# Kernel optimization log

Hardware: AMD Instinct MI355X
Metric: run time of the kernel (lower is better)

Reference implementation:

```python
import jax, jax.numpy as jnp
from jax import lax
import numpy as np
import math

MAXV = 127.0  # 2**(8-1)-1, signed int8 narrow range

def setup_inputs() -> dict:
    key = jax.random.key(0)
    kx, kw, kb = jax.random.split(key, 3)
    B, Cin, H, W = 32, 128, 56, 56
    Cout, K = 256, 3
    x = jax.random.normal(kx, (B, Cin, H, W), dtype=jnp.float32)
    # kaiming_uniform_(a=sqrt(5)) -> bound = sqrt(6 / ((1+5) * fan_in)) = 1/sqrt(fan_in)
    fan_in = Cin * K * K
    bound = 1.0 / math.sqrt(fan_in)
    weight = jax.random.uniform(kw, (Cout, Cin, K, K), dtype=jnp.float32,
                                minval=-bound, maxval=bound)
    bias = jax.random.uniform(kb, (Cout,), dtype=jnp.float32,
                              minval=-bound, maxval=bound)
    return {"x": x, "weight": weight, "bias": bias}

def _quantize_i8(t):
    """Max-calibrated signed 8-bit quantization (fake_quant=False -> integer output)."""
    amax = jnp.max(jnp.abs(t))
    scale = MAXV / amax
    q = jnp.clip(jnp.round(t * scale), -MAXV, MAXV).astype(jnp.int8)
    return q, scale

def reference(x, weight, bias):
    # quantize activations and weights to int8
    qx, sx = _quantize_i8(x)
    qw, sw = _quantize_i8(weight)
    # exact int8 conv with int32 accumulation (systolic exact path), stride=1, pad=1
    out_i32 = lax.conv_general_dilated(
        qx, qw,
        window_strides=(1, 1),
        padding=((1, 1), (1, 1)),
        dimension_numbers=("NCHW", "OIHW", "NCHW"),
        preferred_element_type=jnp.int32,
    )
    # dequantize and add bias
    out = out_i32.astype(jnp.float32) / (sx * sw)
    return out + bias[None, :, None, None]
```

## Files before the change

kernel.cpp:

```cpp
#include <hip/hip_runtime.h>


#define B_    32
#define CIN   128
#define H_    56
#define W_    56
#define COUT  256
#define HP    58
#define WP    58
#define HWP   (H_*W_)
#define NPIX  (B_*HWP)
#define NCHUNK 18
#define WCHUNK 16384
#define BWIN  24576
#define GSTR  3712

typedef int int4v __attribute__((ext_vector_type(4)));

__device__ __forceinline__ void gld_lds16(const void* g, void* l) {
    __builtin_amdgcn_global_load_lds(
        (const __attribute__((address_space(1))) unsigned int*)g,
        (__attribute__((address_space(3))) unsigned int*)l, 16, 0, 0);
}

__global__ __launch_bounds__(256) void amax_kernel(const float4* __restrict__ x, long n4x,
                                                   const float4* __restrict__ wt, long n4w,
                                                   unsigned* __restrict__ scales) {
    const float4* p; long n4; unsigned* slot; long start, stride;
    if (blockIdx.x < 2048) {
        p = x; n4 = n4x; slot = scales;
        start = (long)blockIdx.x * 256 + threadIdx.x; stride = 2048L * 256;
    } else {
        p = wt; n4 = n4w; slot = scales + 1;
        start = (long)(blockIdx.x - 2048) * 256 + threadIdx.x; stride = 128L * 256;
    }
    float m = 0.f;
    for (long i = start; i < n4; i += stride) {
        float4 v = p[i];
        m = fmaxf(m, fmaxf(fmaxf(fabsf(v.x), fabsf(v.y)), fmaxf(fabsf(v.z), fabsf(v.w))));
    }
    __shared__ float red[256];
    red[threadIdx.x] = m; __syncthreads();
    for (int s = 128; s > 0; s >>= 1) {
        if (threadIdx.x < s) red[threadIdx.x] = fmaxf(red[threadIdx.x], red[threadIdx.x + s]);
        __syncthreads();
    }
    if (threadIdx.x == 0) atomicMax(slot, __float_as_uint(red[0]));
}

__global__ __launch_bounds__(256) void quant_x_kernel(const float* __restrict__ x,
        const unsigned* __restrict__ scales, signed char* __restrict__ xq) {
    const int bh = blockIdx.x;
    const int b = bh / H_, h = bh % H_;
    const float sx = 127.0f / __uint_as_float(scales[0]);
    __shared__ int ldsq[W_ * 33];
    const int tid = threadIdx.x;

    int4 z; z.x = 0; z.y = 0; z.z = 0; z.w = 0;
    int4* prow = (int4*)(xq + ((long)b * HP + h + 1) * WP * CIN);
    if (tid < 8) prow[tid] = z;
    else if (tid < 16) prow[456 + tid - 8] = z;
    if (h == 0) {
        int4* r0 = (int4*)(xq + (long)b * HP * WP * CIN);
        for (int i = tid; i < 464; i += 256) r0[i] = z;
    } else if (h == H_ - 1) {
        int4* rt = (int4*)(xq + ((long)b * HP + 57) * WP * CIN);
        for (int i = tid; i < 464; i += 256) rt[i] = z;
    }

    const int w = tid & 63;
    const int chi = tid >> 6;
    if (w < W_) {
        const float* xb = x + (long)b * CIN * HWP + h * W_ + w;
#pragma unroll
        for (int it = 0; it < 8; ++it) {
            const int c4 = it * 4 + chi;
            int pk = 0;
#pragma unroll
            for (int u = 0; u < 4; ++u) {
                float v = xb[(long)(c4 * 4 + u) * HWP];
                float q = fminf(127.f, fmaxf(-127.f, rintf(v * sx)));
                pk |= ((int)q & 0xff) << (u * 8);
            }
            ldsq[w * 33 + c4] = pk;
        }
    }
    __syncthreads();
    int4* dst = (int4*)(xq + (((long)b * HP + h + 1) * WP + 1) * CIN);
    for (int idx = tid; idx < W_ * 8; idx += 256) {
        const int ww = idx >> 3, c16 = idx & 7;
        int4 v;
        v.x = ldsq[ww * 33 + c16 * 4 + 0];
        v.y = ldsq[ww * 33 + c16 * 4 + 1];
        v.z = ldsq[ww * 33 + c16 * 4 + 2];
        v.w = ldsq[ww * 33 + c16 * 4 + 3];
        dst[ww * 8 + c16] = v;
    }
}

__global__ __launch_bounds__(256) void quant_w_kernel(const float* __restrict__ wt,
        const unsigned* __restrict__ scales, signed char* __restrict__ wq) {
    const int id = blockIdx.x * 256 + threadIdx.x;
    if (id >= COUT * 9 * 32) return;
    const float sw = 127.0f / __uint_as_float(scales[1]);
    const int co = id / 288;
    const int r  = id % 288;
    const int t  = r / 32;
    const int c4 = r % 32;
    int pk = 0;
#pragma unroll
    for (int u = 0; u < 4; ++u) {
        float v = wt[(co * CIN + c4 * 4 + u) * 9 + t];
        float q = fminf(127.f, fmaxf(-127.f, rintf(v * sw)));
        pk |= ((int)q & 0xff) << (u * 8);
    }
    const int k = t * CIN + c4 * 4;
    const int chunk = k >> 6;
    const int o = k & 63;
    *(int*)(wq + (long)chunk * WCHUNK + (co >> 7) * 8192 +
            (o >> 4) * 2048 + (co & 127) * 16 + (o & 15)) = pk;
}

__global__ __launch_bounds__(256, 3) void conv_kernel(
        const signed char* __restrict__ xq, const signed char* __restrict__ wq,
        const float* __restrict__ bias, const unsigned* __restrict__ scales,
        float* __restrict__ out) {
    __shared__ signed char smem[54272];

    const int tid = threadIdx.x;
    const int lane = tid & 63;
    const int wv = tid >> 6;
    const int ln = lane & 15;
    const int g  = lane >> 4;

    const int bid = blockIdx.x;
    const int wg  = (bid & 7) * 224 + (bid >> 3);
    const int pxt = wg >> 1;
    const int cot = wg & 1;
    const int px_blk = pxt * 112;
    const int cotoff = cot * 8192;

    const int b0 = pxt / 28;
    const int h0 = (pxt % 28) * 2;

    const int aoff0 = wv * 1024 + lane * 16;
    const int aoff1 = aoff0 + 4096;

    int px58v[7];
#pragma unroll
    for (int j = 0; j < 7; ++j) {
        const int pl = j * 16 + ln;
        px58v[j] = pl + (pl >= 56 ? 2 : 0);
    }

    const signed char* win = xq + (long)(b0 * HP + h0) * WP * CIN;
    int4v wbuf[8];
#pragma unroll
    for (int k = 0; k < 8; ++k) {
        const int u = tid + k * 256;
        if (u < 1856) wbuf[k] = *(const int4v*)(win + u * 16);
    }
#pragma unroll
    for (int k = 0; k < 8; ++k) {
        const int u = tid + k * 256;
        if (u < 1856)
            *(int4v*)&smem[BWIN + (u & 7) * GSTR + (u >> 3) * 16] = wbuf[k];
    }

#define STAGE_A(c) { const int bf_ = (c) % 3; \
    gld_lds16(wq + (c) * WCHUNK + cotoff + aoff0, &smem[bf_ * 8192 + aoff0]); \
    gld_lds16(wq + (c) * WCHUNK + cotoff + aoff1, &smem[bf_ * 8192 + aoff1]); }

    STAGE_A(0);
    STAGE_A(1);
    asm volatile("s_waitcnt lgkmcnt(0)" ::: "memory");

#define TAP58(c) ((((c) >> 1) / 3) * 58 + (((c) >> 1) % 3))
#define LDA_(i) (*(const int4v*)&smem[buf * 8192 + g * 2048 + (wv * 32 + (i) * 16 + ln) * 16])
#define LDB_(c, j) (*(const int4v*)&smem[BWIN + (((c) & 1) * 4 + g) * GSTR + (px58v[j] + TAP58(c)) * 16])
#define MM(i, j, A, Bv) acc[i][j] = __builtin_amdgcn_mfma_i32_16x16x64_i8(A, Bv, acc[i][j], 0, 0, 0)

#define CHUNK(c, VM) { \
    const int buf = (c) % 3; \
    asm volatile("s_waitcnt vmcnt(" #VM ")\n\ts_barrier" ::: "memory"); \
    if ((c) + 2 < NCHUNK) STAGE_A((c) + 2); \
    int4v Bf0 = LDB_(c, 0), Bf1 = LDB_(c, 1), Bf2 = LDB_(c, 2), Bf3 = LDB_(c, 3); \
    int4v Bf4 = LDB_(c, 4), Bf5 = LDB_(c, 5), Bf6 = LDB_(c, 6); \
    int4v Af0 = LDA_(0), Af1 = LDA_(1); \
    __builtin_amdgcn_s_setprio(1); \
    MM(0, 0, Af0, Bf0); MM(1, 0, Af1, Bf0); MM(0, 1, Af0, Bf1); MM(1, 1, Af1, Bf1); \
    MM(0, 2, Af0, Bf2); MM(1, 2, Af1, Bf2); MM(0, 3, Af0, Bf3); MM(1, 3, Af1, Bf3); \
    MM(0, 4, Af0, Bf4); MM(1, 4, Af1, Bf4); MM(0, 5, Af0, Bf5); MM(1, 5, Af1, Bf5); \
    MM(0, 6, Af0, Bf6); MM(1, 6, Af1, Bf6); \
    __builtin_amdgcn_s_setprio(0); }

    int4v acc[2][7] = {};
    CHUNK(0,  2) CHUNK(1,  2) CHUNK(2,  2) CHUNK(3,  2) CHUNK(4,  2) CHUNK(5,  2)
    CHUNK(6,  2) CHUNK(7,  2) CHUNK(8,  2) CHUNK(9,  2) CHUNK(10, 2) CHUNK(11, 2)
    CHUNK(12, 2) CHUNK(13, 2) CHUNK(14, 2) CHUNK(15, 2) CHUNK(16, 2) CHUNK(17, 0)
#undef CHUNK
#undef MM
#undef LDB_
#undef LDA_
#undef TAP58
#undef STAGE_A

    const float ax = __uint_as_float(scales[0]);
    const float aw = __uint_as_float(scales[1]);
    const float inv = 1.0f / ((127.0f / ax) * (127.0f / aw));

    __syncthreads();
    float* ldsT = (float*)smem;

#pragma unroll
    for (int rnd = 0; rnd < 4; ++rnd) {
        if (wv == rnd) {
#pragma unroll
            for (int i = 0; i < 2; ++i)
#pragma unroll
                for (int r = 0; r < 4; ++r) {
                    const int cl = i * 16 + g * 4 + r;
#pragma unroll
                    for (int j = 0; j < 7; ++j)
                        ldsT[cl * 116 + j * 16 + ln] = (float)acc[i][j][r] * inv;
                }
        }
        __syncthreads();
#pragma unroll
        for (int it = 0; it < 4; ++it) {
            const int idx = it * 256 + tid;
            if (idx < 896) {
                const int row = idx / 28, c4 = idx - row * 28;
                const int co = cot * 128 + rnd * 32 + row;
                float4 v = *(float4*)&ldsT[row * 116 + c4 * 4];
                const float bsv = bias[co];
                v.x += bsv; v.y += bsv; v.z += bsv; v.w += bsv;
                *(float4*)&out[((long)b0 * COUT + co) * HWP + h0 * 56 + c4 * 4] = v;
            }
        }
        if (rnd < 3) __syncthreads();
    }
}

extern "C" void kernel_launch(void* const* d_in, const int* in_sizes, int n_in,
                              void* d_out, int out_size, void* d_ws, size_t ws_size,
                              hipStream_t stream) {
    const float* x  = (const float*)d_in[0];
    const float* wt = (const float*)d_in[1];
    const float* bs = (const float*)d_in[2];
    float* out = (float*)d_out;

    unsigned* scales = (unsigned*)d_ws;
    const size_t XQ_OFF   = 256;
    const size_t XQ_BYTES = (size_t)B_ * HP * WP * CIN;
    signed char* xq = (signed char*)d_ws + XQ_OFF;
    signed char* wq = xq + XQ_BYTES;

    hipMemsetAsync(d_ws, 0, 8, stream);

    const long n4x = (long)B_ * CIN * H_ * W_ / 4;
    const long n4w = (long)COUT * CIN * 9 / 4;
    amax_kernel<<<2176, 256, 0, stream>>>((const float4*)x, n4x, (const float4*)wt, n4w, scales);

    quant_x_kernel<<<B_ * H_, 256, 0, stream>>>(x, scales, xq);
    quant_w_kernel<<<(COUT * 9 * 32 + 255) / 256, 256, 0, stream>>>(wt, scales, wq);

    conv_kernel<<<2 * NPIX / 112, 256, 0, stream>>>(xq, wq, bs, scales, out);
}
```

Baseline: 221.5 us.

## Widen conv tile to all 256 output channels per block

Each workgroup now computes all 256 output channels for its 112-pixel tile instead of splitting channels across two blocks, so the im2col input window is loaded once rather than twice. The weight chunk staged per stage doubles and each wave holds 4x7 accumulators. LDS grows to about 79KB and occupancy drops to 2 blocks per CU, and register pressure rises. The group stride is padded slightly, which shifts the LDS bank mapping of the input window.

```diff
diff --git a/kernel.cpp b/kernel.cpp
--- a/kernel.cpp
+++ b/kernel.cpp
@@ -12,8 +12,8 @@
 #define NPIX  (B_*HWP)
 #define NCHUNK 18
 #define WCHUNK 16384
-#define BWIN  24576
-#define GSTR  3712
+#define BWIN  49152
+#define GSTR  3728
 
 typedef int int4v __attribute__((ext_vector_type(4)));
 
@@ -121,11 +121,11 @@
             (o >> 4) * 2048 + (co & 127) * 16 + (o & 15)) = pk;
 }
 
-__global__ __launch_bounds__(256, 3) void conv_kernel(
+__global__ __launch_bounds__(256, 2) void conv_kernel(
         const signed char* __restrict__ xq, const signed char* __restrict__ wq,
         const float* __restrict__ bias, const unsigned* __restrict__ scales,
         float* __restrict__ out) {
-    __shared__ signed char smem[54272];
+    __shared__ signed char smem[78976];
 
     const int tid = threadIdx.x;
     const int lane = tid & 63;
@@ -134,17 +134,11 @@
     const int g  = lane >> 4;
 
     const int bid = blockIdx.x;
-    const int wg  = (bid & 7) * 224 + (bid >> 3);
-    const int pxt = wg >> 1;
-    const int cot = wg & 1;
-    const int px_blk = pxt * 112;
-    const int cotoff = cot * 8192;
-
-    const int b0 = pxt / 28;
-    const int h0 = (pxt % 28) * 2;
-
-    const int aoff0 = wv * 1024 + lane * 16;
-    const int aoff1 = aoff0 + 4096;
+    const int wg  = (bid & 7) * 112 + (bid >> 3);
+    const int b0 = wg / 28;
+    const int h0 = (wg % 28) * 2;
+
+    const int koff = wv * 1024 + lane * 16;
 
     int px58v[7];
 #pragma unroll
@@ -168,15 +162,19 @@
     }
 
 #define STAGE_A(c) { const int bf_ = (c) % 3; \
-    gld_lds16(wq + (c) * WCHUNK + cotoff + aoff0, &smem[bf_ * 8192 + aoff0]); \
-    gld_lds16(wq + (c) * WCHUNK + cotoff + aoff1, &smem[bf_ * 8192 + aoff1]); }
+    gld_lds16(wq + (c) * WCHUNK + koff,         &smem[bf_ * 16384 + koff]); \
+    gld_lds16(wq + (c) * WCHUNK + koff + 4096,  &smem[bf_ * 16384 + koff + 4096]); \
+    gld_lds16(wq + (c) * WCHUNK + koff + 8192,  &smem[bf_ * 16384 + koff + 8192]); \
+    gld_lds16(wq + (c) * WCHUNK + koff + 12288, &smem[bf_ * 16384 + koff + 12288]); }
 
     STAGE_A(0);
+    __builtin_amdgcn_sched_barrier(0);
     STAGE_A(1);
     asm volatile("s_waitcnt lgkmcnt(0)" ::: "memory");
 
 #define TAP58(c) ((((c) >> 1) / 3) * 58 + (((c) >> 1) % 3))
-#define LDA_(i) (*(const int4v*)&smem[buf * 8192 + g * 2048 + (wv * 32 + (i) * 16 + ln) * 16])
+#define LDA_(i) (*(const int4v*)&smem[buf * 16384 + (wv >> 1) * 8192 + g * 2048 + \
+                                      ((wv & 1) * 64 + (i) * 16 + ln) * 16])
 #define LDB_(c, j) (*(const int4v*)&smem[BWIN + (((c) & 1) * 4 + g) * GSTR + (px58v[j] + TAP58(c)) * 16])
 #define MM(i, j, A, Bv) acc[i][j] = __builtin_amdgcn_mfma_i32_16x16x64_i8(A, Bv, acc[i][j], 0, 0, 0)
 
@@ -186,18 +184,21 @@
     if ((c) + 2 < NCHUNK) STAGE_A((c) + 2); \
     int4v Bf0 = LDB_(c, 0), Bf1 = LDB_(c, 1), Bf2 = LDB_(c, 2), Bf3 = LDB_(c, 3); \
     int4v Bf4 = LDB_(c, 4), Bf5 = LDB_(c, 5), Bf6 = LDB_(c, 6); \
-    int4v Af0 = LDA_(0), Af1 = LDA_(1); \
+    int4v Af0 = LDA_(0), Af1 = LDA_(1), Af2 = LDA_(2), Af3 = LDA_(3); \
     __builtin_amdgcn_s_setprio(1); \
-    MM(0, 0, Af0, Bf0); MM(1, 0, Af1, Bf0); MM(0, 1, Af0, Bf1); MM(1, 1, Af1, Bf1); \
-    MM(0, 2, Af0, Bf2); MM(1, 2, Af1, Bf2); MM(0, 3, Af0, Bf3); MM(1, 3, Af1, Bf3); \
-    MM(0, 4, Af0, Bf4); MM(1, 4, Af1, Bf4); MM(0, 5, Af0, Bf5); MM(1, 5, Af1, Bf5); \
-    MM(0, 6, Af0, Bf6); MM(1, 6, Af1, Bf6); \
+    MM(0, 0, Af0, Bf0); MM(1, 0, Af1, Bf0); MM(2, 0, Af2, Bf0); MM(3, 0, Af3, Bf0); \
+    MM(0, 1, Af0, Bf1); MM(1, 1, Af1, Bf1); MM(2, 1, Af2, Bf1); MM(3, 1, Af3, Bf1); \
+    MM(0, 2, Af0, Bf2); MM(1, 2, Af1, Bf2); MM(2, 2, Af2, Bf2); MM(3, 2, Af3, Bf2); \
+    MM(0, 3, Af0, Bf3); MM(1, 3, Af1, Bf3); MM(2, 3, Af2, Bf3); MM(3, 3, Af3, Bf3); \
+    MM(0, 4, Af0, Bf4); MM(1, 4, Af1, Bf4); MM(2, 4, Af2, Bf4); MM(3, 4, Af3, Bf4); \
+    MM(0, 5, Af0, Bf5); MM(1, 5, Af1, Bf5); MM(2, 5, Af2, Bf5); MM(3, 5, Af3, Bf5); \
+    MM(0, 6, Af0, Bf6); MM(1, 6, Af1, Bf6); MM(2, 6, Af2, Bf6); MM(3, 6, Af3, Bf6); \
     __builtin_amdgcn_s_setprio(0); }
 
-    int4v acc[2][7] = {};
-    CHUNK(0,  2) CHUNK(1,  2) CHUNK(2,  2) CHUNK(3,  2) CHUNK(4,  2) CHUNK(5,  2)
-    CHUNK(6,  2) CHUNK(7,  2) CHUNK(8,  2) CHUNK(9,  2) CHUNK(10, 2) CHUNK(11, 2)
-    CHUNK(12, 2) CHUNK(13, 2) CHUNK(14, 2) CHUNK(15, 2) CHUNK(16, 2) CHUNK(17, 0)
+    int4v acc[4][7] = {};
+    CHUNK(0,  4) CHUNK(1,  4) CHUNK(2,  4) CHUNK(3,  4) CHUNK(4,  4) CHUNK(5,  4)
+    CHUNK(6,  4) CHUNK(7,  4) CHUNK(8,  4) CHUNK(9,  4) CHUNK(10, 4) CHUNK(11, 4)
+    CHUNK(12, 4) CHUNK(13, 4) CHUNK(14, 4) CHUNK(15, 4) CHUNK(16, 4) CHUNK(17, 0)
 #undef CHUNK
 #undef MM
 #undef LDB_
@@ -216,7 +217,7 @@
     for (int rnd = 0; rnd < 4; ++rnd) {
         if (wv == rnd) {
 #pragma unroll
-            for (int i = 0; i < 2; ++i)
+            for (int i = 0; i < 4; ++i)
 #pragma unroll
                 for (int r = 0; r < 4; ++r) {
                     const int cl = i * 16 + g * 4 + r;
@@ -227,16 +228,14 @@
         }
         __syncthreads();
 #pragma unroll
-        for (int it = 0; it < 4; ++it) {
+        for (int it = 0; it < 7; ++it) {
             const int idx = it * 256 + tid;
-            if (idx < 896) {
-                const int row = idx / 28, c4 = idx - row * 28;
-                const int co = cot * 128 + rnd * 32 + row;
-                float4 v = *(float4*)&ldsT[row * 116 + c4 * 4];
-                const float bsv = bias[co];
-                v.x += bsv; v.y += bsv; v.z += bsv; v.w += bsv;
-                *(float4*)&out[((long)b0 * COUT + co) * HWP + h0 * 56 + c4 * 4] = v;
-            }
+            const int row = idx / 28, c4 = idx - row * 28;
+            const int co = rnd * 64 + row;
+            float4 v = *(float4*)&ldsT[row * 116 + c4 * 4];
+            const float bsv = bias[co];
+            v.x += bsv; v.y += bsv; v.z += bsv; v.w += bsv;
+            *(float4*)&out[((long)b0 * COUT + co) * HWP + h0 * 56 + c4 * 4] = v;
         }
         if (rnd < 3) __syncthreads();
     }
@@ -265,5 +264,5 @@
     quant_x_kernel<<<B_ * H_, 256, 0, stream>>>(x, scales, xq);
     quant_w_kernel<<<(COUT * 9 * 32 + 255) / 256, 256, 0, stream>>>(wt, scales, wq);
 
-    conv_kernel<<<2 * NPIX / 112, 256, 0, stream>>>(xq, wq, bs, scales, out);
-}
+    conv_kernel<<<NPIX / 112, 256, 0, stream>>>(xq, wq, bs, scales, out);
+}
```

New measurement: 211.8 us. -4.4%, faster.
